# Optimization experiments

Measured on AMD Instinct MI355X. Metric: run time of the kernel, lower is better.

The kernel has to match this reference:

```python
import jax, jax.numpy as jnp
import numpy as np

B, L, D, H, E = 2, 2048, 1024, 4096, 8
CAP = int(1.25 * 2 * (B * L) / E)  # top-2 capacity = 1280


def setup_inputs() -> dict:
    key = jax.random.key(0)
    k0, k1, k2, k3 = jax.random.split(key, 4)
    gate_std = (0.1 / D) ** 0.5
    return {
        "inputs": jax.random.normal(k0, (B, L, D), jnp.float32),
        "gate_weight": jax.random.normal(k1, (E, D), jnp.float32) * gate_std,
        "w1": jax.random.normal(k2, (E, D, H), jnp.float32) * 0.02,
        "b1": jnp.zeros((E, 1, H), jnp.float32),
        "w2": jax.random.normal(k3, (E, H, D), jnp.float32) * 0.02,
        "b2": jnp.zeros((E, 1, D), jnp.float32),
    }


def reference(inputs, gate_weight, w1, b1, w2, b2):
    tokens = inputs.reshape(-1, D)                      # [S, D], S = B*L
    # gate computed in fp32 as in original
    logits = tokens.astype(jnp.float32) @ gate_weight.astype(jnp.float32).T  # [S, E]
    gates = jax.nn.softmax(logits, axis=-1)

    # top-2 routing
    top1 = jnp.argmax(gates, axis=-1)
    mask1 = jax.nn.one_hot(top1, E, dtype=jnp.float32)  # [S, E]
    gates_wo1 = jnp.where(mask1 > 0, -jnp.inf, gates)
    top2 = jnp.argmax(gates_wo1, axis=-1)
    mask2 = jax.nn.one_hot(top2, E, dtype=jnp.float32)

    # load-balancing aux loss (GShard style, pre-capacity masks)
    me = jnp.mean(gates, axis=0)
    ce = jnp.mean(mask1, axis=0)
    l_aux = E * jnp.sum(me * ce)

    # capacity positions via cumulative sum per expert
    loc1 = jnp.cumsum(mask1, axis=0) - 1.0              # [S, E]
    loc2 = jnp.cumsum(mask2, axis=0) - 1.0 + jnp.sum(mask1, axis=0, keepdims=True)
    mask1 = mask1 * (loc1 < CAP)
    mask2 = mask2 * (loc2 < CAP)

    gate1 = jnp.sum(gates * mask1, axis=-1)             # [S]
    gate2 = jnp.sum(gates * mask2, axis=-1)
    denom = jnp.maximum(gate1 + gate2, jnp.finfo(jnp.float32).eps)
    wgt1 = gate1 / denom
    wgt2 = gate2 / denom

    pos1 = jnp.sum(loc1 * mask1, axis=-1).astype(jnp.int32)  # [S]
    pos2 = jnp.sum(loc2 * mask2, axis=-1).astype(jnp.int32)
    cap1 = jax.nn.one_hot(pos1, CAP, dtype=jnp.float32)      # [S, C]
    cap2 = jax.nn.one_hot(pos2, CAP, dtype=jnp.float32)

    # combine weights [S, E, C] and dispatch mask
    combine = (wgt1[:, None, None] * mask1[:, :, None] * cap1[:, None, :]
               + wgt2[:, None, None] * mask2[:, :, None] * cap2[:, None, :])
    sec_mask_f = (combine > 0).astype(inputs.dtype)

    # dispatch: [E, C, S] @ [S, D] -> [E, C, D]
    dispatch = jnp.einsum('sec,sd->ecd', sec_mask_f, tokens)

    # per-expert FFN (batched over experts)
    h = jax.nn.gelu(jnp.einsum('ecd,edh->ech', dispatch, w1) + b1)
    expert_out = jnp.einsum('ech,ehd->ecd', h, w2) + b2

    # combine: [S, E*C] @ [E*C, D] -> [S, D]
    ans = jnp.einsum('sec,ecd->sd', combine.astype(inputs.dtype), expert_out)
    return ans.reshape(inputs.shape), l_aux
```

## Files before the change

### kernel.cpp

```cpp
#include <hip/hip_runtime.h>

#define S_TOK 4096
#define DMODEL 1024
#define HDIM 4096
#define NEXP 8
#define CAPACITY 1280

struct TokenRoute { int e1, p1, e2, p2; float w1, w2; };

typedef __bf16 bf16x8 __attribute__((ext_vector_type(8)));
typedef float f32x4 __attribute__((ext_vector_type(4)));

__device__ __forceinline__ unsigned short f2bf(float f) {
    unsigned int u = __float_as_uint(f);
    unsigned int r = 0x7fffu + ((u >> 16) & 1u);
    return (unsigned short)((u + r) >> 16);
}
__device__ __forceinline__ float bf2f(unsigned short b) {
    return __uint_as_float(((unsigned int)b) << 16);
}

__device__ __forceinline__ void gload16(const void* gsrc, void* ldst) {
    __builtin_amdgcn_global_load_lds(
        (const __attribute__((address_space(1))) unsigned int*)gsrc,
        (__attribute__((address_space(3))) unsigned int*)ldst, 16, 0, 0);
}

__device__ __forceinline__ float gelu_tanh(float x) {
    float u = 0.7978845608028654f * (x + 0.044715f * x * x * x);
    return 0.5f * x * (1.0f + tanhf(u));
}

__global__ void transpose_cvt(const float* __restrict__ src, unsigned short* __restrict__ dst,
                              int R, int C) {
    __shared__ unsigned short t[64][68];
    size_t eoff = (size_t)blockIdx.z * R * C;
    src += eoff; dst += eoff;
    int r0 = blockIdx.y * 64, c0 = blockIdx.x * 64;
    int tid = threadIdx.x;
    int rr = tid >> 2, q = tid & 3;
#pragma unroll
    for (int s = 0; s < 4; ++s) {
        const float4 v = *(const float4*)(src + (size_t)(r0 + rr) * C + c0 + q * 16 + s * 4);
        int cc = q * 16 + s * 4;
        t[rr][cc + 0] = f2bf(v.x); t[rr][cc + 1] = f2bf(v.y);
        t[rr][cc + 2] = f2bf(v.z); t[rr][cc + 3] = f2bf(v.w);
    }
    __syncthreads();
#pragma unroll
    for (int s = 0; s < 4; ++s) {
        int rb = q * 16 + s * 4;
        ushort4 o;
        o.x = t[rb + 0][rr]; o.y = t[rb + 1][rr]; o.z = t[rb + 2][rr]; o.w = t[rb + 3][rr];
        *(ushort4*)(dst + (size_t)(c0 + rr) * R + r0 + rb) = o;
    }
}

__global__ void gate_kernel(const float* __restrict__ tokens, const float* __restrict__ gw,
                            float* __restrict__ gates, TokenRoute* __restrict__ route) {
    int s = blockIdx.x, l = threadIdx.x;
    const float* x = tokens + (size_t)s * DMODEL;
    float p[NEXP];
#pragma unroll
    for (int e = 0; e < NEXP; ++e) p[e] = 0.f;
#pragma unroll
    for (int it = 0; it < 4; ++it) {
        int i = (it * 64 + l) * 4;
        float4 v = *(const float4*)(x + i);
#pragma unroll
        for (int e = 0; e < NEXP; ++e) {
            float4 g = *(const float4*)(gw + e * DMODEL + i);
            p[e] += v.x * g.x + v.y * g.y + v.z * g.z + v.w * g.w;
        }
    }
#pragma unroll
    for (int e = 0; e < NEXP; ++e) {
        float v = p[e];
        v += __shfl_xor(v, 32); v += __shfl_xor(v, 16); v += __shfl_xor(v, 8);
        v += __shfl_xor(v, 4);  v += __shfl_xor(v, 2);  v += __shfl_xor(v, 1);
        p[e] = v;
    }
    int e1 = 0; float b1v = p[0];
#pragma unroll
    for (int e = 1; e < NEXP; ++e) if (p[e] > b1v) { b1v = p[e]; e1 = e; }
    int e2 = -1; float b2v = -3.0e38f;
#pragma unroll
    for (int e = 0; e < NEXP; ++e) if (e != e1 && p[e] > b2v) { b2v = p[e]; e2 = e; }
    float mx = p[0];
#pragma unroll
    for (int e = 1; e < NEXP; ++e) mx = fmaxf(mx, p[e]);
    float sum = 0.f;
#pragma unroll
    for (int e = 0; e < NEXP; ++e) { p[e] = __expf(p[e] - mx); sum += p[e]; }
    float inv = 1.0f / sum;
#pragma unroll
    for (int e = 0; e < NEXP; ++e) p[e] *= inv;
    float g1 = __expf(b1v - mx) * inv;
    float g2 = __expf(b2v - mx) * inv;
    if (l == 0) {
        float* gp = gates + (size_t)s * NEXP;
#pragma unroll
        for (int e = 0; e < NEXP; ++e) gp[e] = p[e];
        TokenRoute r; r.e1 = e1; r.p1 = 0; r.e2 = e2; r.p2 = 0; r.w1 = g1; r.w2 = g2;
        route[s] = r;
    }
}

__global__ void route_scan(TokenRoute* __restrict__ route, const float* __restrict__ gates,
                           int* __restrict__ cnt, float* __restrict__ laux_out) {
    __shared__ unsigned int buf[1024][NEXP];
    int t = threadIdx.x;
    int te1[4], te2[4]; float tg1[4], tg2[4];
    unsigned int c1[NEXP], c2[NEXP];
#pragma unroll
    for (int e = 0; e < NEXP; ++e) { c1[e] = 0; c2[e] = 0; }
    for (int j = 0; j < 4; ++j) {
        TokenRoute r = route[t * 4 + j];
        te1[j] = r.e1; te2[j] = r.e2; tg1[j] = r.w1; tg2[j] = r.w2;
#pragma unroll
        for (int e = 0; e < NEXP; ++e) { c1[e] += (r.e1 == e); c2[e] += (r.e2 == e); }
    }
#pragma unroll
    for (int e = 0; e < NEXP; ++e) buf[t][e] = c1[e];
    __syncthreads();
    for (int off = 1; off < 1024; off <<= 1) {
        unsigned int v[NEXP];
#pragma unroll
        for (int e = 0; e < NEXP; ++e) v[e] = (t >= off) ? buf[t - off][e] : 0u;
        __syncthreads();
#pragma unroll
        for (int e = 0; e < NEXP; ++e) buf[t][e] += v[e];
        __syncthreads();
    }
    unsigned int ex1[NEXP], tot1[NEXP];
#pragma unroll
    for (int e = 0; e < NEXP; ++e) { ex1[e] = buf[t][e] - c1[e]; tot1[e] = buf[1023][e]; }
    __syncthreads();
#pragma unroll
    for (int e = 0; e < NEXP; ++e) buf[t][e] = c2[e];
    __syncthreads();
    for (int off = 1; off < 1024; off <<= 1) {
        unsigned int v[NEXP];
#pragma unroll
        for (int e = 0; e < NEXP; ++e) v[e] = (t >= off) ? buf[t - off][e] : 0u;
        __syncthreads();
#pragma unroll
        for (int e = 0; e < NEXP; ++e) buf[t][e] += v[e];
        __syncthreads();
    }
    unsigned int ex2[NEXP], tot2[NEXP];
#pragma unroll
    for (int e = 0; e < NEXP; ++e) { ex2[e] = buf[t][e] - c2[e]; tot2[e] = buf[1023][e]; }
    __syncthreads();
    float gs[NEXP];
#pragma unroll
    for (int e = 0; e < NEXP; ++e) gs[e] = 0.f;
    for (int j = 0; j < 4; ++j) {
        const float* gp = gates + (size_t)(t * 4 + j) * NEXP;
#pragma unroll
        for (int e = 0; e < NEXP; ++e) gs[e] += gp[e];
    }
    float* fb = (float*)&buf[0][0];
#pragma unroll
    for (int e = 0; e < NEXP; ++e) fb[t * NEXP + e] = gs[e];
    __syncthreads();
    for (int off = 512; off > 0; off >>= 1) {
        if (t < off) {
#pragma unroll
            for (int e = 0; e < NEXP; ++e) fb[t * NEXP + e] += fb[(t + off) * NEXP + e];
        }
        __syncthreads();
    }
    if (t == 0) {
        float laux = 0.f;
#pragma unroll
        for (int e = 0; e < NEXP; ++e) {
            laux += (fb[e] / (float)S_TOK) * ((float)tot1[e] / (float)S_TOK);
            int c = (int)(tot1[e] + tot2[e]);
            cnt[e] = c < CAPACITY ? c : CAPACITY;
        }
        *laux_out = laux * (float)NEXP;
    }
    unsigned int r1[NEXP], r2[NEXP];
#pragma unroll
    for (int e = 0; e < NEXP; ++e) { r1[e] = 0; r2[e] = 0; }
    for (int j = 0; j < 4; ++j) {
        int E1 = te1[j], E2 = te2[j];
        unsigned int loc1 = 0, loc2 = 0;
#pragma unroll
        for (int e = 0; e < NEXP; ++e) if (E1 == e) { loc1 = ex1[e] + r1[e]; r1[e]++; }
#pragma unroll
        for (int e = 0; e < NEXP; ++e) if (E2 == e) { loc2 = ex2[e] + r2[e] + tot1[e]; r2[e]++; }
        bool k1 = loc1 < CAPACITY, k2 = loc2 < CAPACITY;
        float G1 = k1 ? tg1[j] : 0.f;
        float G2 = k2 ? tg2[j] : 0.f;
        float denom = fmaxf(G1 + G2, 1.1920929e-07f);
        TokenRoute r;
        r.e1 = E1; r.p1 = k1 ? (int)loc1 : -1;
        r.e2 = E2; r.p2 = k2 ? (int)loc2 : -1;
        r.w1 = G1 / denom; r.w2 = G2 / denom;
        route[t * 4 + j] = r;
    }
}

__global__ void dispatch_scatter(const float* __restrict__ tokens, const TokenRoute* __restrict__ route,
                                 unsigned short* __restrict__ disp) {
    int s = blockIdx.x, l = threadIdx.x;
    TokenRoute r = route[s];
    const float* x = tokens + (size_t)s * DMODEL;
    ushort4 vals[4];
#pragma unroll
    for (int q = 0; q < 4; ++q) {
        float4 v = *(const float4*)(x + (q * 64 + l) * 4);
        vals[q].x = f2bf(v.x); vals[q].y = f2bf(v.y); vals[q].z = f2bf(v.z); vals[q].w = f2bf(v.w);
    }
    if (r.p1 >= 0) {
        unsigned short* d = disp + ((size_t)r.e1 * CAPACITY + r.p1) * DMODEL;
#pragma unroll
        for (int q = 0; q < 4; ++q) *(ushort4*)(d + (q * 64 + l) * 4) = vals[q];
    }
    if (r.p2 >= 0) {
        unsigned short* d = disp + ((size_t)r.e2 * CAPACITY + r.p2) * DMODEL;
#pragma unroll
        for (int q = 0; q < 4; ++q) *(ushort4*)(d + (q * 64 + l) * 4) = vals[q];
    }
}

template <int MODE>
__global__ __launch_bounds__(256)
void gemm_bt(const unsigned short* __restrict__ A, const unsigned short* __restrict__ Bt,
             unsigned short* __restrict__ C, const float* __restrict__ bias,
             const int* __restrict__ cnt,
             int N, int K, int Ntiles,
             size_t strideAe, size_t strideBe, size_t strideCe, int biasStride) {
    int e = blockIdx.z;
    int mt = blockIdx.x / Ntiles, nt = blockIdx.x % Ntiles;
    if (mt * 128 >= cnt[e]) return;
    const unsigned short* Ae = A + (size_t)e * strideAe;
    const unsigned short* Be = Bt + (size_t)e * strideBe;
    unsigned short* Ce = C + (size_t)e * strideCe;
    const float* be = bias + (size_t)e * biasStride;

    __shared__ unsigned short sA[2][4096];
    __shared__ unsigned short sB[2][4096];

    int tid = threadIdx.x;
    int w = tid >> 6, lane = tid & 63;
    int wm = w >> 1, wn = w & 1;
    int lr = lane & 15, kc = lane >> 4;
    int srow = lane >> 2, scp = lane & 3;

    f32x4 acc[4][4];
#pragma unroll
    for (int m = 0; m < 4; ++m)
#pragma unroll
        for (int n = 0; n < 4; ++n) acc[m][n] = (f32x4){0.f, 0.f, 0.f, 0.f};

    int nk = K >> 5;
    int swz = ((lr ^ (lr >> 2)) & 3);
    int fA = (wm * 64 + lr) * 32 + ((kc ^ swz) * 8);
    int fB = (wn * 64 + lr) * 32 + ((kc ^ swz) * 8);

    auto stage = [&](int bufi, int kt) {
#pragma unroll
        for (int p = 0; p < 2; ++p) {
            int inst = w * 2 + p;
            int row = inst * 16 + srow;
            int c = scp ^ ((row ^ (row >> 2)) & 3);
            const unsigned short* ga = Ae + (size_t)(mt * 128 + row) * K + kt * 32 + c * 8;
            gload16(ga, &sA[bufi][inst * 512]);
            const unsigned short* gb = Be + (size_t)(nt * 128 + row) * K + kt * 32 + c * 8;
            gload16(gb, &sB[bufi][inst * 512]);
        }
    };

    stage(0, 0);
    int buf = 0;
    for (int kt = 0; kt < nk; ++kt) {
        __syncthreads();
        if (kt + 1 < nk) stage(buf ^ 1, kt + 1);
        bf16x8 av[4], bv[4];
#pragma unroll
        for (int m = 0; m < 4; ++m) av[m] = *(const bf16x8*)&sA[buf][fA + m * 512];
#pragma unroll
        for (int n = 0; n < 4; ++n) bv[n] = *(const bf16x8*)&sB[buf][fB + n * 512];
#pragma unroll
        for (int m = 0; m < 4; ++m)
#pragma unroll
            for (int n = 0; n < 4; ++n)
                acc[m][n] = __builtin_amdgcn_mfma_f32_16x16x32_bf16(av[m], bv[n], acc[m][n], 0, 0, 0);
        buf ^= 1;
    }

    int orow0 = mt * 128 + wm * 64 + (lane >> 4) * 4;
    int ocol0 = nt * 128 + wn * 64 + lr;
#pragma unroll
    for (int m = 0; m < 4; ++m) {
#pragma unroll
        for (int n = 0; n < 4; ++n) {
            int col = ocol0 + n * 16;
            float bvv = be[col];
#pragma unroll
            for (int r = 0; r < 4; ++r) {
                int row = orow0 + m * 16 + r;
                float v = acc[m][n][r] + bvv;
                if (MODE == 0) v = gelu_tanh(v);
                Ce[(size_t)row * N + col] = f2bf(v);
            }
        }
    }
}

__global__ void combine_kernel(const TokenRoute* __restrict__ route, const unsigned short* __restrict__ eout,
                               float* __restrict__ out) {
    int s = blockIdx.x, l = threadIdx.x;
    TokenRoute r = route[s];
    bool v1 = r.p1 >= 0, v2 = r.p2 >= 0;
#pragma unroll
    for (int q = 0; q < 4; ++q) {
        int i = (q * 64 + l) * 4;
        float4 a = {0.f, 0.f, 0.f, 0.f};
        if (v1) {
            const unsigned short* p = eout + ((size_t)r.e1 * CAPACITY + r.p1) * DMODEL + i;
            ushort4 u = *(const ushort4*)p;
            a.x += r.w1 * bf2f(u.x); a.y += r.w1 * bf2f(u.y);
            a.z += r.w1 * bf2f(u.z); a.w += r.w1 * bf2f(u.w);
        }
        if (v2) {
            const unsigned short* p = eout + ((size_t)r.e2 * CAPACITY + r.p2) * DMODEL + i;
            ushort4 u = *(const ushort4*)p;
            a.x += r.w2 * bf2f(u.x); a.y += r.w2 * bf2f(u.y);
            a.z += r.w2 * bf2f(u.z); a.w += r.w2 * bf2f(u.w);
        }
        *(float4*)(out + (size_t)s * DMODEL + i) = a;
    }
}

extern "C" void kernel_launch(void* const* d_in, const int* in_sizes, int n_in,
                              void* d_out, int out_size, void* d_ws, size_t ws_size,
                              hipStream_t stream) {
    const float* inputs = (const float*)d_in[0];
    const float* gw     = (const float*)d_in[1];
    const float* w1     = (const float*)d_in[2];
    const float* b1     = (const float*)d_in[3];
    const float* w2     = (const float*)d_in[4];
    const float* b2     = (const float*)d_in[5];
    float* out = (float*)d_out;

    char* ws = (char*)d_ws;
    const size_t SZ_W = (size_t)NEXP * DMODEL * HDIM * 2;
    const size_t SZ_DISP = (size_t)NEXP * CAPACITY * DMODEL * 2;
    const size_t SZ_H = (size_t)NEXP * CAPACITY * HDIM * 2;
    unsigned short* wb1t = (unsigned short*)(ws);
    unsigned short* wb2t = (unsigned short*)(ws + SZ_W);
    unsigned short* disp = (unsigned short*)(ws + 2 * SZ_W);
    unsigned short* h    = (unsigned short*)(ws + 2 * SZ_W + SZ_DISP);
    float* gates = (float*)(ws + 2 * SZ_W + SZ_DISP + SZ_H);
    TokenRoute* route = (TokenRoute*)(ws + 2 * SZ_W + SZ_DISP + SZ_H + (size_t)S_TOK * NEXP * 4);
    int* cnt = (int*)((char*)route + (size_t)S_TOK * sizeof(TokenRoute));

    transpose_cvt<<<dim3(HDIM / 64, DMODEL / 64, NEXP), 256, 0, stream>>>(w1, wb1t, DMODEL, HDIM);
    transpose_cvt<<<dim3(DMODEL / 64, HDIM / 64, NEXP), 256, 0, stream>>>(w2, wb2t, HDIM, DMODEL);
    gate_kernel<<<S_TOK, 64, 0, stream>>>(inputs, gw, gates, route);
    route_scan<<<1, 1024, 0, stream>>>(route, gates, cnt, out + (size_t)S_TOK * DMODEL);
    hipMemsetAsync(disp, 0, SZ_DISP, stream);
    dispatch_scatter<<<S_TOK, 64, 0, stream>>>(inputs, route, disp);
    gemm_bt<0><<<dim3((CAPACITY / 128) * (HDIM / 128), 1, NEXP), 256, 0, stream>>>(
        disp, wb1t, h, b1, cnt, HDIM, DMODEL, HDIM / 128,
        (size_t)CAPACITY * DMODEL, (size_t)HDIM * DMODEL, (size_t)CAPACITY * HDIM, HDIM);
    gemm_bt<1><<<dim3((CAPACITY / 128) * (DMODEL / 128), 1, NEXP), 256, 0, stream>>>(
        h, wb2t, disp, b2, cnt, DMODEL, HDIM, DMODEL / 128,
        (size_t)CAPACITY * HDIM, (size_t)DMODEL * HDIM, (size_t)CAPACITY * DMODEL, DMODEL);
    combine_kernel<<<S_TOK, 64, 0, stream>>>(route, disp, out);
}
```

Baseline: 628.6 us.

## Rewrite expert GEMMs with 256-row tiles, 512 threads, deeper K pipeline

The expert GEMM kernel is replaced by a templated 256-row-tile version with 512 threads and BK=64. It uses two-stage LDS buffering with explicit vmcnt waits and barriers, raised MFMA priority, and an LDS-staged epilogue that writes 16-byte vector stores. Several other changes come with it: a faster sigmoid-form GELU, wave-shuffle packed-counter scans in route_scan, vectorised 8-wide stores in the weight transpose, and removal of the dispatch-buffer memset. The larger tiles and bigger LDS footprint aim to raise arithmetic intensity and cut global traffic, at the cost of fewer resident blocks and coarser skipping of tiles past each expert's token count.

```diff
diff --git a/kernel.cpp b/kernel.cpp
--- a/kernel.cpp
+++ b/kernel.cpp
@@ -10,6 +10,7 @@
 
 typedef __bf16 bf16x8 __attribute__((ext_vector_type(8)));
 typedef float f32x4 __attribute__((ext_vector_type(4)));
+typedef unsigned short ushort8v __attribute__((ext_vector_type(8)));
 
 __device__ __forceinline__ unsigned short f2bf(float f) {
     unsigned int u = __float_as_uint(f);
@@ -26,33 +27,39 @@
         (__attribute__((address_space(3))) unsigned int*)ldst, 16, 0, 0);
 }
 
-__device__ __forceinline__ float gelu_tanh(float x) {
-    float u = 0.7978845608028654f * (x + 0.044715f * x * x * x);
-    return 0.5f * x * (1.0f + tanhf(u));
+template <int N> __device__ __forceinline__ void wait_vmcnt() {
+    if constexpr (N == 0) asm volatile("s_waitcnt vmcnt(0)" ::: "memory");
+    else if constexpr (N == 6) asm volatile("s_waitcnt vmcnt(6)" ::: "memory");
+    else if constexpr (N == 8) asm volatile("s_waitcnt vmcnt(8)" ::: "memory");
+}
+
+__device__ __forceinline__ float gelu_f(float x) {
+    float u = x * (0.7978845608028654f + 0.0356774081363f * x * x);
+    return x / (1.0f + __expf(-2.0f * u));
 }
 
 __global__ void transpose_cvt(const float* __restrict__ src, unsigned short* __restrict__ dst,
                               int R, int C) {
-    __shared__ unsigned short t[64][68];
+    __shared__ unsigned short t[64][66];
     size_t eoff = (size_t)blockIdx.z * R * C;
-    src += eoff; dst += eoff;
-    int r0 = blockIdx.y * 64, c0 = blockIdx.x * 64;
-    int tid = threadIdx.x;
-    int rr = tid >> 2, q = tid & 3;
-#pragma unroll
-    for (int s = 0; s < 4; ++s) {
-        const float4 v = *(const float4*)(src + (size_t)(r0 + rr) * C + c0 + q * 16 + s * 4);
-        int cc = q * 16 + s * 4;
-        t[rr][cc + 0] = f2bf(v.x); t[rr][cc + 1] = f2bf(v.y);
-        t[rr][cc + 2] = f2bf(v.z); t[rr][cc + 3] = f2bf(v.w);
+    int r0 = blockIdx.y * 64, c0 = blockIdx.x * 64, tid = threadIdx.x;
+    int rr = tid >> 4, cq = (tid & 15) * 4;
+#pragma unroll
+    for (int p = 0; p < 4; ++p) {
+        int row = p * 16 + rr;
+        float4 v = *(const float4*)(src + eoff + (size_t)(r0 + row) * C + c0 + cq);
+        t[row][cq + 0] = f2bf(v.x); t[row][cq + 1] = f2bf(v.y);
+        t[row][cq + 2] = f2bf(v.z); t[row][cq + 3] = f2bf(v.w);
     }
     __syncthreads();
-#pragma unroll
-    for (int s = 0; s < 4; ++s) {
-        int rb = q * 16 + s * 4;
-        ushort4 o;
-        o.x = t[rb + 0][rr]; o.y = t[rb + 1][rr]; o.z = t[rb + 2][rr]; o.w = t[rb + 3][rr];
-        *(ushort4*)(dst + (size_t)(c0 + rr) * R + r0 + rb) = o;
+    int k0 = (tid & 7) * 8;
+#pragma unroll
+    for (int pp = 0; pp < 2; ++pp) {
+        int oc = pp * 32 + (tid >> 3);
+        ushort8v o;
+#pragma unroll
+        for (int x = 0; x < 8; ++x) o[x] = t[k0 + x][oc];
+        *(ushort8v*)(dst + eoff + (size_t)(c0 + oc) * R + r0 + k0) = o;
     }
 }
 
@@ -106,98 +113,103 @@
     }
 }
 
-__global__ void route_scan(TokenRoute* __restrict__ route, const float* __restrict__ gates,
-                           int* __restrict__ cnt, float* __restrict__ laux_out) {
-    __shared__ unsigned int buf[1024][NEXP];
-    int t = threadIdx.x;
-    int te1[4], te2[4]; float tg1[4], tg2[4];
-    unsigned int c1[NEXP], c2[NEXP];
-#pragma unroll
-    for (int e = 0; e < NEXP; ++e) { c1[e] = 0; c2[e] = 0; }
+__device__ __forceinline__ unsigned ext16(unsigned long long lo, unsigned long long hi, int e) {
+    unsigned long long q = (e < 4) ? lo : hi;
+    return (unsigned)((q >> ((e & 3) * 16)) & 0xFFFFULL);
+}
+
+__global__ __launch_bounds__(1024)
+void route_scan(TokenRoute* __restrict__ route, const float* __restrict__ gates,
+                int* __restrict__ cnt, float* __restrict__ laux_out) {
+    __shared__ unsigned long long wt[16][4];
+    __shared__ float fsum[16][NEXP];
+    int t = threadIdx.x, wid = t >> 6, ln = t & 63;
+    TokenRoute tr[4];
+    unsigned long long own[4] = {0, 0, 0, 0};
+#pragma unroll
     for (int j = 0; j < 4; ++j) {
-        TokenRoute r = route[t * 4 + j];
-        te1[j] = r.e1; te2[j] = r.e2; tg1[j] = r.w1; tg2[j] = r.w2;
-#pragma unroll
-        for (int e = 0; e < NEXP; ++e) { c1[e] += (r.e1 == e); c2[e] += (r.e2 == e); }
-    }
-#pragma unroll
-    for (int e = 0; e < NEXP; ++e) buf[t][e] = c1[e];
+        tr[j] = route[t * 4 + j];
+        int e1 = tr[j].e1, e2 = tr[j].e2;
+        if (e1 < 4) own[0] += 1ULL << (e1 * 16); else own[1] += 1ULL << ((e1 - 4) * 16);
+        if (e2 < 4) own[2] += 1ULL << (e2 * 16); else own[3] += 1ULL << ((e2 - 4) * 16);
+    }
+    unsigned long long inc[4] = {own[0], own[1], own[2], own[3]};
+#pragma unroll
+    for (int off = 1; off < 64; off <<= 1) {
+#pragma unroll
+        for (int q = 0; q < 4; ++q) {
+            unsigned long long v = __shfl_up(inc[q], off);
+            if (ln >= off) inc[q] += v;
+        }
+    }
+    if (ln == 63) {
+#pragma unroll
+        for (int q = 0; q < 4; ++q) wt[wid][q] = inc[q];
+    }
     __syncthreads();
-    for (int off = 1; off < 1024; off <<= 1) {
-        unsigned int v[NEXP];
-#pragma unroll
-        for (int e = 0; e < NEXP; ++e) v[e] = (t >= off) ? buf[t - off][e] : 0u;
-        __syncthreads();
-#pragma unroll
-        for (int e = 0; e < NEXP; ++e) buf[t][e] += v[e];
-        __syncthreads();
-    }
-    unsigned int ex1[NEXP], tot1[NEXP];
-#pragma unroll
-    for (int e = 0; e < NEXP; ++e) { ex1[e] = buf[t][e] - c1[e]; tot1[e] = buf[1023][e]; }
-    __syncthreads();
-#pragma unroll
-    for (int e = 0; e < NEXP; ++e) buf[t][e] = c2[e];
-    __syncthreads();
-    for (int off = 1; off < 1024; off <<= 1) {
-        unsigned int v[NEXP];
-#pragma unroll
-        for (int e = 0; e < NEXP; ++e) v[e] = (t >= off) ? buf[t - off][e] : 0u;
-        __syncthreads();
-#pragma unroll
-        for (int e = 0; e < NEXP; ++e) buf[t][e] += v[e];
-        __syncthreads();
-    }
-    unsigned int ex2[NEXP], tot2[NEXP];
-#pragma unroll
-    for (int e = 0; e < NEXP; ++e) { ex2[e] = buf[t][e] - c2[e]; tot2[e] = buf[1023][e]; }
-    __syncthreads();
+    unsigned long long woff[4] = {0, 0, 0, 0}, tot[4] = {0, 0, 0, 0};
+    for (int w = 0; w < 16; ++w) {
+#pragma unroll
+        for (int q = 0; q < 4; ++q) {
+            unsigned long long v = wt[w][q];
+            tot[q] += v;
+            if (w < wid) woff[q] += v;
+        }
+    }
+    unsigned long long ex[4];
+#pragma unroll
+    for (int q = 0; q < 4; ++q) ex[q] = woff[q] + inc[q] - own[q];
+
     float gs[NEXP];
 #pragma unroll
     for (int e = 0; e < NEXP; ++e) gs[e] = 0.f;
+#pragma unroll
     for (int j = 0; j < 4; ++j) {
         const float* gp = gates + (size_t)(t * 4 + j) * NEXP;
 #pragma unroll
         for (int e = 0; e < NEXP; ++e) gs[e] += gp[e];
     }
-    float* fb = (float*)&buf[0][0];
-#pragma unroll
-    for (int e = 0; e < NEXP; ++e) fb[t * NEXP + e] = gs[e];
+#pragma unroll
+    for (int e = 0; e < NEXP; ++e) {
+        float v = gs[e];
+        v += __shfl_xor(v, 32); v += __shfl_xor(v, 16); v += __shfl_xor(v, 8);
+        v += __shfl_xor(v, 4);  v += __shfl_xor(v, 2);  v += __shfl_xor(v, 1);
+        gs[e] = v;
+    }
+    if (ln == 0) {
+#pragma unroll
+        for (int e = 0; e < NEXP; ++e) fsum[wid][e] = gs[e];
+    }
     __syncthreads();
-    for (int off = 512; off > 0; off >>= 1) {
-        if (t < off) {
-#pragma unroll
-            for (int e = 0; e < NEXP; ++e) fb[t * NEXP + e] += fb[(t + off) * NEXP + e];
-        }
-        __syncthreads();
-    }
     if (t == 0) {
         float laux = 0.f;
 #pragma unroll
         for (int e = 0; e < NEXP; ++e) {
-            laux += (fb[e] / (float)S_TOK) * ((float)tot1[e] / (float)S_TOK);
-            int c = (int)(tot1[e] + tot2[e]);
+            float m = 0.f;
+            for (int w = 0; w < 16; ++w) m += fsum[w][e];
+            unsigned t1 = ext16(tot[0], tot[1], e);
+            unsigned t2 = ext16(tot[2], tot[3], e);
+            laux += (m / (float)S_TOK) * ((float)t1 / (float)S_TOK);
+            int c = (int)(t1 + t2);
             cnt[e] = c < CAPACITY ? c : CAPACITY;
         }
         *laux_out = laux * (float)NEXP;
     }
-    unsigned int r1[NEXP], r2[NEXP];
-#pragma unroll
-    for (int e = 0; e < NEXP; ++e) { r1[e] = 0; r2[e] = 0; }
+    unsigned long long r1lo = ex[0], r1hi = ex[1], r2lo = ex[2], r2hi = ex[3];
+#pragma unroll
     for (int j = 0; j < 4; ++j) {
-        int E1 = te1[j], E2 = te2[j];
-        unsigned int loc1 = 0, loc2 = 0;
-#pragma unroll
-        for (int e = 0; e < NEXP; ++e) if (E1 == e) { loc1 = ex1[e] + r1[e]; r1[e]++; }
-#pragma unroll
-        for (int e = 0; e < NEXP; ++e) if (E2 == e) { loc2 = ex2[e] + r2[e] + tot1[e]; r2[e]++; }
+        int e1 = tr[j].e1, e2 = tr[j].e2;
+        unsigned loc1 = ext16(r1lo, r1hi, e1);
+        if (e1 < 4) r1lo += 1ULL << (e1 * 16); else r1hi += 1ULL << ((e1 - 4) * 16);
+        unsigned loc2 = ext16(r2lo, r2hi, e2) + ext16(tot[0], tot[1], e2);
+        if (e2 < 4) r2lo += 1ULL << (e2 * 16); else r2hi += 1ULL << ((e2 - 4) * 16);
         bool k1 = loc1 < CAPACITY, k2 = loc2 < CAPACITY;
-        float G1 = k1 ? tg1[j] : 0.f;
-        float G2 = k2 ? tg2[j] : 0.f;
+        float G1 = k1 ? tr[j].w1 : 0.f;
+        float G2 = k2 ? tr[j].w2 : 0.f;
         float denom = fmaxf(G1 + G2, 1.1920929e-07f);
         TokenRoute r;
-        r.e1 = E1; r.p1 = k1 ? (int)loc1 : -1;
-        r.e2 = E2; r.p2 = k2 ? (int)loc2 : -1;
+        r.e1 = e1; r.p1 = k1 ? (int)loc1 : -1;
+        r.e2 = e2; r.p2 = k2 ? (int)loc2 : -1;
         r.w1 = G1 / denom; r.w2 = G2 / denom;
         route[t * 4 + j] = r;
     }
@@ -226,88 +238,140 @@
     }
 }
 
-template <int MODE>
-__global__ __launch_bounds__(256)
-void gemm_bt(const unsigned short* __restrict__ A, const unsigned short* __restrict__ Bt,
+template <int BN, int WM, int WN, int MODE>
+__global__ __launch_bounds__(512, 2)
+void gemm256(const unsigned short* __restrict__ A, const unsigned short* __restrict__ Bt,
              unsigned short* __restrict__ C, const float* __restrict__ bias,
              const int* __restrict__ cnt,
              int N, int K, int Ntiles,
              size_t strideAe, size_t strideBe, size_t strideCe, int biasStride) {
+    constexpr int MF = 256 / WM / 16;
+    constexpr int NF = BN / WN / 16;
+    constexpr int RW = 256 / WM;
+    constexpr int CW = BN / WN;
+    constexpr int NBJ = BN / 64;
+    constexpr int LPT = 4 + NBJ;
+    constexpr int ASLOT = 256 * 64;
+    constexpr int BSLOT = BN * 64;
+
+    __shared__ unsigned short slds[(2 * 256 + 2 * BN) * 64];
+
     int e = blockIdx.z;
     int mt = blockIdx.x / Ntiles, nt = blockIdx.x % Ntiles;
-    if (mt * 128 >= cnt[e]) return;
+    if (mt * 256 >= cnt[e]) return;
     const unsigned short* Ae = A + (size_t)e * strideAe;
     const unsigned short* Be = Bt + (size_t)e * strideBe;
     unsigned short* Ce = C + (size_t)e * strideCe;
     const float* be = bias + (size_t)e * biasStride;
 
-    __shared__ unsigned short sA[2][4096];
-    __shared__ unsigned short sB[2][4096];
-
     int tid = threadIdx.x;
-    int w = tid >> 6, lane = tid & 63;
-    int wm = w >> 1, wn = w & 1;
-    int lr = lane & 15, kc = lane >> 4;
-    int srow = lane >> 2, scp = lane & 3;
-
-    f32x4 acc[4][4];
-#pragma unroll
-    for (int m = 0; m < 4; ++m)
-#pragma unroll
-        for (int n = 0; n < 4; ++n) acc[m][n] = (f32x4){0.f, 0.f, 0.f, 0.f};
-
-    int nk = K >> 5;
-    int swz = ((lr ^ (lr >> 2)) & 3);
-    int fA = (wm * 64 + lr) * 32 + ((kc ^ swz) * 8);
-    int fB = (wn * 64 + lr) * 32 + ((kc ^ swz) * 8);
-
-    auto stage = [&](int bufi, int kt) {
-#pragma unroll
-        for (int p = 0; p < 2; ++p) {
-            int inst = w * 2 + p;
-            int row = inst * 16 + srow;
-            int c = scp ^ ((row ^ (row >> 2)) & 3);
-            const unsigned short* ga = Ae + (size_t)(mt * 128 + row) * K + kt * 32 + c * 8;
-            gload16(ga, &sA[bufi][inst * 512]);
-            const unsigned short* gb = Be + (size_t)(nt * 128 + row) * K + kt * 32 + c * 8;
-            gload16(gb, &sB[bufi][inst * 512]);
-        }
+    int wv = tid >> 6, ln = tid & 63;
+    int wm = wv / WN, wn = wv % WN;
+    int lr = ln & 15, kc = ln >> 4;
+    int rsw = lr & 7;
+
+    size_t gOffA[4]; int ldsA[4];
+#pragma unroll
+    for (int j = 0; j < 4; ++j) {
+        int g = (wv * 4 + j) * 64 + ln;
+        int row = g >> 3, cl = g & 7, cs = cl ^ (row & 7);
+        ldsA[j] = (wv * 4 + j) * 512;
+        gOffA[j] = (size_t)(mt * 256 + row) * K + cs * 8;
+    }
+    size_t gOffB[NBJ]; int ldsB[NBJ];
+#pragma unroll
+    for (int j = 0; j < NBJ; ++j) {
+        int g = (wv * NBJ + j) * 64 + ln;
+        int row = g >> 3, cl = g & 7, cs = cl ^ (row & 7);
+        ldsB[j] = (wv * NBJ + j) * 512;
+        gOffB[j] = (size_t)(nt * BN + row) * K + cs * 8;
+    }
+    int aoff[MF], boff[NF];
+#pragma unroll
+    for (int i = 0; i < MF; ++i) aoff[i] = (wm * RW + i * 16 + lr) * 64;
+#pragma unroll
+    for (int j = 0; j < NF; ++j) boff[j] = (wn * CW + j * 16 + lr) * 64;
+    int chk0 = ((kc) ^ rsw) * 8;
+    int chk1 = ((kc + 4) ^ rsw) * 8;
+
+    f32x4 acc[MF][NF];
+#pragma unroll
+    for (int i = 0; i < MF; ++i)
+#pragma unroll
+        for (int j = 0; j < NF; ++j) acc[i][j] = (f32x4){0.f, 0.f, 0.f, 0.f};
+
+    auto stage = [&](int slot, int kt) {
+        unsigned short* da = slds + slot * ASLOT;
+        unsigned short* db = slds + 2 * ASLOT + slot * BSLOT;
+#pragma unroll
+        for (int j = 0; j < 4; ++j) gload16(Ae + gOffA[j] + kt * 64, da + ldsA[j]);
+#pragma unroll
+        for (int j = 0; j < NBJ; ++j) gload16(Be + gOffB[j] + kt * 64, db + ldsB[j]);
     };
 
+    int nk = K >> 6;
     stage(0, 0);
-    int buf = 0;
+    stage(1, 1);
+    wait_vmcnt<LPT>();
+    __builtin_amdgcn_s_barrier();
+
+    int cur = 0;
     for (int kt = 0; kt < nk; ++kt) {
-        __syncthreads();
-        if (kt + 1 < nk) stage(buf ^ 1, kt + 1);
-        bf16x8 av[4], bv[4];
-#pragma unroll
-        for (int m = 0; m < 4; ++m) av[m] = *(const bf16x8*)&sA[buf][fA + m * 512];
-#pragma unroll
-        for (int n = 0; n < 4; ++n) bv[n] = *(const bf16x8*)&sB[buf][fB + n * 512];
-#pragma unroll
-        for (int m = 0; m < 4; ++m)
-#pragma unroll
-            for (int n = 0; n < 4; ++n)
-                acc[m][n] = __builtin_amdgcn_mfma_f32_16x16x32_bf16(av[m], bv[n], acc[m][n], 0, 0, 0);
-        buf ^= 1;
-    }
-
-    int orow0 = mt * 128 + wm * 64 + (lane >> 4) * 4;
-    int ocol0 = nt * 128 + wn * 64 + lr;
-#pragma unroll
-    for (int m = 0; m < 4; ++m) {
-#pragma unroll
-        for (int n = 0; n < 4; ++n) {
-            int col = ocol0 + n * 16;
-            float bvv = be[col];
+        const unsigned short* sa = slds + cur * ASLOT;
+        const unsigned short* sb = slds + 2 * ASLOT + cur * BSLOT;
+        __builtin_amdgcn_s_setprio(1);
+#pragma unroll
+        for (int s = 0; s < 2; ++s) {
+            int ck = (s == 0) ? chk0 : chk1;
+            bf16x8 av[MF], bv[NF];
+#pragma unroll
+            for (int i = 0; i < MF; ++i) av[i] = *(const bf16x8*)(sa + aoff[i] + ck);
+#pragma unroll
+            for (int j = 0; j < NF; ++j) bv[j] = *(const bf16x8*)(sb + boff[j] + ck);
+#pragma unroll
+            for (int i = 0; i < MF; ++i)
+#pragma unroll
+                for (int j = 0; j < NF; ++j)
+                    acc[i][j] = __builtin_amdgcn_mfma_f32_16x16x32_bf16(av[i], bv[j], acc[i][j], 0, 0, 0);
+        }
+        __builtin_amdgcn_s_setprio(0);
+        __builtin_amdgcn_sched_barrier(0);
+        __builtin_amdgcn_s_barrier();
+        if (kt + 2 < nk) stage(cur, kt + 2);
+        if (kt + 1 < nk) {
+            if (kt + 2 < nk) wait_vmcnt<LPT>(); else wait_vmcnt<0>();
+            __builtin_amdgcn_s_barrier();
+        }
+        cur ^= 1;
+    }
+
+    __syncthreads();
+    unsigned short* scratch = slds + wv * (RW * CW);
+    float bvj[NF];
+#pragma unroll
+    for (int j = 0; j < NF; ++j) bvj[j] = be[nt * BN + wn * CW + j * 16 + lr];
+#pragma unroll
+    for (int i = 0; i < MF; ++i) {
+#pragma unroll
+        for (int j = 0; j < NF; ++j) {
+            int col_l = j * 16 + lr;
 #pragma unroll
             for (int r = 0; r < 4; ++r) {
-                int row = orow0 + m * 16 + r;
-                float v = acc[m][n][r] + bvv;
-                if (MODE == 0) v = gelu_tanh(v);
-                Ce[(size_t)row * N + col] = f2bf(v);
+                int row_l = i * 16 + kc * 4 + r;
+                float v = acc[i][j][r] + bvj[j];
+                if (MODE == 0) v = gelu_f(v);
+                scratch[row_l * CW + col_l] = f2bf(v);
             }
         }
+    }
+    int rrow = ln >> 3, rcol = (ln & 7) * 8;
+#pragma unroll
+    for (int p = 0; p < RW / 8; ++p) {
+        int row_l = p * 8 + rrow;
+        ushort8v v = *(const ushort8v*)&scratch[row_l * CW + rcol];
+        int row_g = mt * 256 + wm * RW + row_l;
+        int col_g = nt * BN + wn * CW + rcol;
+        *(ushort8v*)&Ce[(size_t)row_g * N + col_g] = v;
     }
 }
 
@@ -363,12 +427,11 @@
     transpose_cvt<<<dim3(DMODEL / 64, HDIM / 64, NEXP), 256, 0, stream>>>(w2, wb2t, HDIM, DMODEL);
     gate_kernel<<<S_TOK, 64, 0, stream>>>(inputs, gw, gates, route);
     route_scan<<<1, 1024, 0, stream>>>(route, gates, cnt, out + (size_t)S_TOK * DMODEL);
-    hipMemsetAsync(disp, 0, SZ_DISP, stream);
     dispatch_scatter<<<S_TOK, 64, 0, stream>>>(inputs, route, disp);
-    gemm_bt<0><<<dim3((CAPACITY / 128) * (HDIM / 128), 1, NEXP), 256, 0, stream>>>(
-        disp, wb1t, h, b1, cnt, HDIM, DMODEL, HDIM / 128,
+    gemm256<256, 2, 4, 0><<<dim3((CAPACITY / 256 + 1) * (HDIM / 256), 1, NEXP), 512, 0, stream>>>(
+        disp, wb1t, h, b1, cnt, HDIM, DMODEL, HDIM / 256,
         (size_t)CAPACITY * DMODEL, (size_t)HDIM * DMODEL, (size_t)CAPACITY * HDIM, HDIM);
-    gemm_bt<1><<<dim3((CAPACITY / 128) * (DMODEL / 128), 1, NEXP), 256, 0, stream>>>(
+    gemm256<128, 4, 2, 1><<<dim3((CAPACITY / 256 + 1) * (DMODEL / 128), 1, NEXP), 512, 0, stream>>>(
         h, wb2t, disp, b2, cnt, DMODEL, HDIM, DMODEL / 128,
         (size_t)CAPACITY * HDIM, (size_t)DMODEL * HDIM, (size_t)CAPACITY * DMODEL, DMODEL);
     combine_kernel<<<S_TOK, 64, 0, stream>>>(route, disp, out);
```

Measured after the change: 642.5 us. 1.02x slower.
